# Optimization experiments

Measured on AMD Instinct MI355X. Metric: run time of the kernel, lower is better.

## Reference

```python
import jax, jax.numpy as jnp
import numpy as np

B, S, C = 2, 4096, 2048
H, D = 16, 128  # inner_dim = H*D = C
EPS = 1e-15     # processor self.eps
PAD_VAL = 1.0   # processor self.pad_val


def setup_inputs() -> dict:
    key = jax.random.key(0)
    ks = jax.random.split(key, 5)
    scale = C ** -0.5
    x = jax.random.normal(ks[0], (B, S, C), jnp.float32)
    Wq = jax.random.normal(ks[1], (C, C), jnp.float32) * scale
    Wk = jax.random.normal(ks[2], (C, C), jnp.float32) * scale
    Wv = jax.random.normal(ks[3], (C, C), jnp.float32) * scale
    Wo = jax.random.normal(ks[4], (C, C), jnp.float32) * scale
    bq = jnp.zeros((C,), jnp.float32)
    bk = jnp.zeros((C,), jnp.float32)
    bv = jnp.zeros((C,), jnp.float32)
    bo = jnp.zeros((C,), jnp.float32)
    # RoPE tables: pairs are adjacent (x.reshape(..., -1, 2)), so each freq repeats twice
    inv_freq = 1.0 / (10000.0 ** (np.arange(0, D, 2, dtype=np.float32) / D))
    freqs = np.outer(np.arange(S, dtype=np.float32), inv_freq)  # [S, D/2]
    emb = np.repeat(freqs, 2, axis=1)                            # [S, D]
    cos = jnp.asarray(np.cos(emb), jnp.float32)
    sin = jnp.asarray(np.sin(emb), jnp.float32)
    return {"x": x, "cos": cos, "sin": sin, "Wq": Wq, "bq": bq, "Wk": Wk,
            "bk": bk, "Wv": Wv, "bv": bv, "Wo": Wo, "bo": bo}


def _rope(t, cos, sin):
    # t: [B, H, S, D]; cos/sin: [S, D]; adjacent-pair rotation
    tr = t[..., 0::2]
    ti = t[..., 1::2]
    t_rot = jnp.stack([-ti, tr], axis=-1).reshape(t.shape)
    return t * cos + t_rot * sin


def reference(x, cos, sin, Wq, bq, Wk, bk, Wv, bv, Wo, bo):
    # projections -> [B, H, S, D] (matches transpose(-1,-2).reshape(B,H,D,S) split)
    q = (x @ Wq.T + bq).reshape(B, S, H, D).transpose(0, 2, 1, 3)
    k = (x @ Wk.T + bk).reshape(B, S, H, D).transpose(0, 2, 1, 3)
    v = (x @ Wv.T + bv).reshape(B, S, H, D).transpose(0, 2, 1, 3)
    # RoPE on q and k (self-attention), then ReLU feature map
    q = jax.nn.relu(_rope(q, cos, sin))
    k = jax.nn.relu(_rope(k, cos, sin))
    # pad value with ones along head_dim: torch F.pad(value,(0,0,0,1),value=1.0)
    v_pad = jnp.concatenate([v, jnp.full((B, H, S, 1), PAD_VAL, v.dtype)], axis=-1)  # [B,H,S,D+1]
    # linear attention: vk = value @ key  -> [B,H,D+1,D];  hs = vk @ query -> [B,H,D+1,S]
    vk = jnp.einsum('bhsn,bhsd->bhnd', v_pad, k)
    hs = jnp.einsum('bhnd,bhsd->bhns', vk, q)
    # eps-normalize by the padded-ones channel
    hs = hs[:, :, :-1] / (hs[:, :, -1:] + EPS)  # [B,H,D,S]
    out = hs.transpose(0, 3, 1, 2).reshape(B, S, H * D)  # view(B,H*D,S).permute(0,2,1)
    return out @ Wo.T + bo
```

## Files before the change

### kernel.cpp

```cpp
#include <hip/hip_runtime.h>


typedef unsigned short u16;
typedef __attribute__((ext_vector_type(8))) short bf16x8;
typedef __attribute__((ext_vector_type(4))) float f32x4;

__device__ __forceinline__ float bf2f(u16 u) {
    union { unsigned int i; float f; } x; x.i = ((unsigned int)u) << 16; return x.f;
}
__device__ __forceinline__ u16 f2bf(float f) {
    union { unsigned int i; float f; } x; x.f = f;
    unsigned int i = x.i;
    return (u16)((i + 0x7fffu + ((i >> 16) & 1u)) >> 16);
}
__device__ __forceinline__ uint4 pack8(const float* __restrict__ src) {
    float4 f0 = *(const float4*)(src);
    float4 f1 = *(const float4*)(src + 4);
    union { u16 u[8]; uint4 v; } P;
    P.u[0] = f2bf(f0.x); P.u[1] = f2bf(f0.y); P.u[2] = f2bf(f0.z); P.u[3] = f2bf(f0.w);
    P.u[4] = f2bf(f1.x); P.u[5] = f2bf(f1.y); P.u[6] = f2bf(f1.z); P.u[7] = f2bf(f1.w);
    return P.v;
}
__device__ __forceinline__ void gll16(void* lds, const void* g) {
    __builtin_amdgcn_global_load_lds(
        (const __attribute__((address_space(1))) unsigned int*)g,
        (__attribute__((address_space(3))) unsigned int*)lds, 16, 0, 0);
}

__global__ __launch_bounds__(256) void cast_all(
    const float* __restrict__ x,  const float* __restrict__ Wq,
    const float* __restrict__ Wk, const float* __restrict__ Wv,
    const float* __restrict__ Wo,
    u16* __restrict__ Xb, u16* __restrict__ Wqkvb, u16* __restrict__ Wob)
{
    int bid = blockIdx.x, t = threadIdx.x;
    const float* s; u16* d; size_t i;
    if (bid < 8192)       { s = x;  d = Xb;              i = (size_t)bid * 256 + t; }
    else if (bid < 10240) { s = Wq; d = Wqkvb;           i = (size_t)(bid - 8192)  * 256 + t; }
    else if (bid < 12288) { s = Wk; d = Wqkvb + 4194304; i = (size_t)(bid - 10240) * 256 + t; }
    else if (bid < 14336) { s = Wv; d = Wqkvb + 8388608; i = (size_t)(bid - 12288) * 256 + t; }
    else                  { s = Wo; d = Wob;             i = (size_t)(bid - 14336) * 256 + t; }
    *(uint4*)(d + i * 8) = pack8(s + i * 8);
}

__global__ __launch_bounds__(256) void gemm_qkv(
    const u16* __restrict__ Xb, const u16* __restrict__ Wqkvb,
    const float* __restrict__ bq, const float* __restrict__ bk, const float* __restrict__ bv,
    const float* __restrict__ cosT, const float* __restrict__ sinT,
    u16* __restrict__ Q, u16* __restrict__ K, u16* __restrict__ V)
{
    __shared__ __align__(16) u16 As[128 * 32];
    __shared__ __align__(16) u16 Bs[128 * 32];

    int t  = threadIdx.x;
    int bm = blockIdx.x;
    int bn = blockIdx.y;
    int region = bn >> 4;
    const u16*   W    = Wqkvb + (size_t)region * 4194304;
    const float* bias = (region == 0) ? bq : (region == 1 ? bk : bv);
    u16* OUT          = (region == 0) ? Q  : (region == 1 ? K  : V);

    int m0 = bm * 128;
    int n0 = (bn & 15) * 128;

    int w = t >> 6, lane = t & 63, quad = lane >> 4, l16 = lane & 15;
    int wm0 = (w >> 1) * 64, wn0 = (w & 1) * 64;
    int w32 = w * 32;
    int lr  = lane >> 2;
    int lc  = (lane & 3) * 8;

    const u16* ga = Xb + (size_t)(m0 + w32 + lr) * 2048 + lc;
    const u16* gb = W  + (size_t)(n0 + w32 + lr) * 2048 + lc;

    f32x4 acc[4][4] = {};

    for (int k0 = 0; k0 < 2048; k0 += 32) {
        __syncthreads();
        gll16(As + (size_t)w32 * 32,        ga + k0);
        gll16(As + (size_t)(w32 + 16) * 32, ga + k0 + 16 * 2048);
        gll16(Bs + (size_t)w32 * 32,        gb + k0);
        gll16(Bs + (size_t)(w32 + 16) * 32, gb + k0 + 16 * 2048);
        __syncthreads();

        bf16x8 af[4], bfr[4];
#pragma unroll
        for (int i = 0; i < 4; i++) af[i]  = *(const bf16x8*)(As + (wm0 + i * 16 + l16) * 32 + quad * 8);
#pragma unroll
        for (int j = 0; j < 4; j++) bfr[j] = *(const bf16x8*)(Bs + (wn0 + j * 16 + l16) * 32 + quad * 8);
#pragma unroll
        for (int i = 0; i < 4; i++)
#pragma unroll
            for (int j = 0; j < 4; j++)
                acc[i][j] = __builtin_amdgcn_mfma_f32_16x16x32_bf16(af[i], bfr[j], acc[i][j], 0, 0, 0);
    }

#pragma unroll
    for (int i = 0; i < 4; i++) {
#pragma unroll
        for (int j = 0; j < 4; j++) {
            int nc   = n0 + wn0 + j * 16 + l16;
            int h    = nc >> 7, dpos = nc & 127;
            float bia = bias[nc];
#pragma unroll
            for (int r = 0; r < 4; r++) {
                int mr = m0 + wm0 + i * 16 + quad * 4 + r;
                int b  = mr >> 12, s = mr & 4095;
                float val = acc[i][j][r] + bia;
                if (region < 2) {
                    float pair = __shfl_xor(val, 1, 64);
                    float c  = cosT[s * 128 + dpos];
                    float sn = sinT[s * 128 + dpos];
                    val = fmaxf(val * c + ((dpos & 1) ? pair : -pair) * sn, 0.f);
                }
                OUT[((size_t)(b * 16 + h) * 4096 + s) * 128 + dpos] = f2bf(val);
            }
        }
    }
}

__global__ __launch_bounds__(256) void ksum_kernel(
    const u16* __restrict__ Kb, float* __restrict__ ksumbuf)
{
    int bh = blockIdx.x, sc8 = blockIdx.y, t = threadIdx.x;
    int dpair = (t & 63) * 2, sq = t >> 6;
    const u16* base = Kb + (size_t)bh * 524288 + (size_t)(sc8 * 512 + sq * 128) * 128 + dpair;
    float s0 = 0.f, s1 = 0.f;
#pragma unroll 8
    for (int r = 0; r < 128; r++) {
        unsigned int wv = *(const unsigned int*)(base + (size_t)r * 128);
        s0 += bf2f((u16)(wv & 0xffff));
        s1 += bf2f((u16)(wv >> 16));
    }
    __shared__ float red[4][128];
    red[sq][dpair]     = s0;
    red[sq][dpair + 1] = s1;
    __syncthreads();
    if (t < 128) {
        float tot = red[0][t] + red[1][t] + red[2][t] + red[3][t];
        atomicAdd(&ksumbuf[bh * 128 + t], tot);
    }
}

__global__ __launch_bounds__(256) void vk_mfma(
    const u16* __restrict__ Kb, const u16* __restrict__ Vb, float* __restrict__ part)
{
    int bh = blockIdx.x;
    int sk = blockIdx.y;
    int t  = threadIdx.x;
    int s0 = sk * 512;

    __shared__ __align__(16) u16 Kt[128 * 32];
    __shared__ __align__(16) u16 Vt[128 * 32];

    const u16* Kp = Kb + (size_t)bh * 524288;
    const u16* Vp = Vb + (size_t)bh * 524288;

    int dgrp  = t & 15;
    int d0    = dgrp * 8;
    int spair = (t >> 4) * 2;
    int sg    = spair >> 3;

    int w = t >> 6, lane = t & 63, quad = lane >> 4, l16 = lane & 15;
    int nbase = (w >> 1) * 64, dbase = (w & 1) * 64;

    f32x4 acc[4][4] = {};

    for (int tile = 0; tile < 16; tile++) {
        int st = s0 + tile * 32;
        __syncthreads();
        {
            const u16* kg = Kp + (size_t)(st + spair) * 128 + d0;
            const u16* vg = Vp + (size_t)(st + spair) * 128 + d0;
            union { uint4 v; u16 u[8]; } ka, kb, va, vb;
            ka.v = *(const uint4*)kg;  kb.v = *(const uint4*)(kg + 128);
            va.v = *(const uint4*)vg;  vb.v = *(const uint4*)(vg + 128);
            int swz = (((sg + dgrp) & 3) << 3) + (spair & 7);
#pragma unroll
            for (int i = 0; i < 8; i++) {
                int e = (d0 + i) * 32 + swz;
                *(unsigned int*)(Kt + e) = (unsigned int)ka.u[i] | ((unsigned int)kb.u[i] << 16);
                *(unsigned int*)(Vt + e) = (unsigned int)va.u[i] | ((unsigned int)vb.u[i] << 16);
            }
        }
        __syncthreads();

        bf16x8 af[4], bfr[4];
#pragma unroll
        for (int i = 0; i < 4; i++) {
            int r = nbase + i * 16 + l16;
            af[i] = *(const bf16x8*)(Vt + r * 32 + (((quad + (r >> 3)) & 3) << 3));
        }
#pragma unroll
        for (int j = 0; j < 4; j++) {
            int r = dbase + j * 16 + l16;
            bfr[j] = *(const bf16x8*)(Kt + r * 32 + (((quad + (r >> 3)) & 3) << 3));
        }
#pragma unroll
        for (int i = 0; i < 4; i++)
#pragma unroll
            for (int j = 0; j < 4; j++)
                acc[i][j] = __builtin_amdgcn_mfma_f32_16x16x32_bf16(af[i], bfr[j], acc[i][j], 0, 0, 0);
    }

    float* dst = part + (size_t)(bh * 8 + sk) * 16384;
#pragma unroll
    for (int i = 0; i < 4; i++) {
#pragma unroll
        for (int j = 0; j < 4; j++) {
#pragma unroll
            for (int r = 0; r < 4; r++) {
                int n = nbase + i * 16 + quad * 4 + r;
                int d = dbase + j * 16 + l16;
                dst[n * 128 + d] = acc[i][j][r];
            }
        }
    }
}

__global__ __launch_bounds__(256) void vk_reduce(const float* __restrict__ part,
                                                 u16* __restrict__ vkb)
{
    int bh = blockIdx.x, by = blockIdx.y, t = threadIdx.x;
    int end = (by + 1) * 2048;
    for (int idx = by * 2048 + t; idx < end; idx += 256) {
        float s = 0.f;
#pragma unroll
        for (int p = 0; p < 8; p++) s += part[(size_t)(bh * 8 + p) * 16384 + idx];
        vkb[(size_t)bh * 16384 + idx] = f2bf(s);
    }
}

__global__ __launch_bounds__(256) void hs_mfma(
    const u16* __restrict__ Qb, const u16* __restrict__ vkb,
    const float* __restrict__ ksumbuf, u16* __restrict__ HS)
{
    int bh = blockIdx.x, sc = blockIdx.y;
    __shared__ __align__(16) u16 qL[128 * 136];
    __shared__ __align__(16) u16 vkL[128 * 136];
    __shared__ float rdL[128];
    __shared__ float ksumL[128];
    int t = threadIdx.x;

    const u16* Qp   = Qb  + ((size_t)bh * 4096 + sc * 128) * 128;
    const u16* vsrc = vkb + (size_t)bh * 16384;
    int row = t >> 4, colc = (t & 15) * 8;
#pragma unroll
    for (int r8 = 0; r8 < 8; r8++) {
        int rr = row + r8 * 16;
        *(uint4*)(qL  + rr * 136 + colc) = *(const uint4*)(Qp   + (size_t)rr * 128 + colc);
        *(uint4*)(vkL + rr * 136 + colc) = *(const uint4*)(vsrc + (size_t)rr * 128 + colc);
    }
    if (t < 128) ksumL[t] = ksumbuf[bh * 128 + t];
    __syncthreads();

    {
        int srow = t >> 1, half = t & 1;
        const u16*   q  = qL + srow * 136 + half * 64;
        const float* kp = ksumL + half * 64;
        float p = 0.f;
#pragma unroll 8
        for (int d = 0; d < 64; d += 4) {
            ushort4 qv = *(const ushort4*)(q + d);
            p += bf2f(qv.x) * kp[d] + bf2f(qv.y) * kp[d + 1]
               + bf2f(qv.z) * kp[d + 2] + bf2f(qv.w) * kp[d + 3];
        }
        p += __shfl_xor(p, 1, 64);
        if (half == 0) rdL[srow] = 1.0f / (p + 1e-15f);
    }

    int w = t >> 6, lane = t & 63, quad = lane >> 4, l16 = lane & 15;
    int wm0 = (w >> 1) * 64, wn0 = (w & 1) * 64;
    f32x4 acc[4][4] = {};
#pragma unroll
    for (int ks = 0; ks < 4; ks++) {
        bf16x8 af[4], bfr[4];
#pragma unroll
        for (int i = 0; i < 4; i++) af[i]  = *(const bf16x8*)(qL  + (wm0 + i * 16 + l16) * 136 + ks * 32 + quad * 8);
#pragma unroll
        for (int j = 0; j < 4; j++) bfr[j] = *(const bf16x8*)(vkL + (wn0 + j * 16 + l16) * 136 + ks * 32 + quad * 8);
#pragma unroll
        for (int i = 0; i < 4; i++)
#pragma unroll
            for (int j = 0; j < 4; j++)
                acc[i][j] = __builtin_amdgcn_mfma_f32_16x16x32_bf16(af[i], bfr[j], acc[i][j], 0, 0, 0);
    }
    __syncthreads();

    int b = bh >> 4, h = bh & 15;
#pragma unroll
    for (int i = 0; i < 4; i++) {
#pragma unroll
        for (int j = 0; j < 4; j++) {
#pragma unroll
            for (int r = 0; r < 4; r++) {
                int sl = wm0 + i * 16 + quad * 4 + r;
                int n  = wn0 + j * 16 + l16;
                size_t srow = (size_t)b * 4096 + sc * 128 + sl;
                HS[srow * 2048 + h * 128 + n] = f2bf(acc[i][j][r] * rdL[sl]);
            }
        }
    }
}

__global__ __launch_bounds__(256) void gemm_out(
    const u16* __restrict__ HSm, const u16* __restrict__ Wob,
    const float* __restrict__ bo, float* __restrict__ OUT)
{
    __shared__ __align__(16) u16 As[128 * 32];
    __shared__ __align__(16) u16 Bs[128 * 32];

    int t  = threadIdx.x;
    int m0 = blockIdx.x * 128;
    int n0 = blockIdx.y * 128;

    int w = t >> 6, lane = t & 63, quad = lane >> 4, l16 = lane & 15;
    int wm0 = (w >> 1) * 64, wn0 = (w & 1) * 64;
    int w32 = w * 32;
    int lr  = lane >> 2;
    int lc  = (lane & 3) * 8;

    const u16* ga = HSm + (size_t)(m0 + w32 + lr) * 2048 + lc;
    const u16* gb = Wob + (size_t)(n0 + w32 + lr) * 2048 + lc;

    f32x4 acc[4][4] = {};

    for (int k0 = 0; k0 < 2048; k0 += 32) {
        __syncthreads();
        gll16(As + (size_t)w32 * 32,        ga + k0);
        gll16(As + (size_t)(w32 + 16) * 32, ga + k0 + 16 * 2048);
        gll16(Bs + (size_t)w32 * 32,        gb + k0);
        gll16(Bs + (size_t)(w32 + 16) * 32, gb + k0 + 16 * 2048);
        __syncthreads();

        bf16x8 af[4], bfr[4];
#pragma unroll
        for (int i = 0; i < 4; i++) af[i]  = *(const bf16x8*)(As + (wm0 + i * 16 + l16) * 32 + quad * 8);
#pragma unroll
        for (int j = 0; j < 4; j++) bfr[j] = *(const bf16x8*)(Bs + (wn0 + j * 16 + l16) * 32 + quad * 8);
#pragma unroll
        for (int i = 0; i < 4; i++)
#pragma unroll
            for (int j = 0; j < 4; j++)
                acc[i][j] = __builtin_amdgcn_mfma_f32_16x16x32_bf16(af[i], bfr[j], acc[i][j], 0, 0, 0);
    }

#pragma unroll
    for (int i = 0; i < 4; i++) {
#pragma unroll
        for (int j = 0; j < 4; j++) {
            int nc = n0 + wn0 + j * 16 + l16;
            float bia = bo[nc];
#pragma unroll
            for (int r = 0; r < 4; r++) {
                int mr = m0 + wm0 + i * 16 + quad * 4 + r;
                OUT[(size_t)mr * 2048 + nc] = acc[i][j][r] + bia;
            }
        }
    }
}

extern "C" void kernel_launch(void* const* d_in, const int* in_sizes, int n_in,
                              void* d_out, int out_size, void* d_ws, size_t ws_size,
                              hipStream_t stream) {
    const float* x    = (const float*)d_in[0];
    const float* cosT = (const float*)d_in[1];
    const float* sinT = (const float*)d_in[2];
    const float* Wq   = (const float*)d_in[3];
    const float* bq   = (const float*)d_in[4];
    const float* Wk   = (const float*)d_in[5];
    const float* bk   = (const float*)d_in[6];
    const float* Wv   = (const float*)d_in[7];
    const float* bv   = (const float*)d_in[8];
    const float* Wo   = (const float*)d_in[9];
    const float* bo   = (const float*)d_in[10];

    char* ws = (char*)d_ws;
    u16*   Wqkvb   = (u16*)(ws);
    u16*   Wob     = (u16*)(ws + 25165824);
    u16*   Xb      = (u16*)(ws + 33554432);
    float* part    = (float*)(ws + 33554432);
    u16*   V       = (u16*)(ws + 67108864);
    u16*   HS      = V;
    u16*   vkb     = (u16*)(ws + 100663296);
    float* ksumbuf = (float*)(ws + 101711872);

    u16* Q  = (u16*)d_out;
    u16* Kb = (u16*)d_out + 16777216;

    hipMemsetAsync(ksumbuf, 0, 32 * 128 * sizeof(float), stream);
    cast_all<<<16384, 256, 0, stream>>>(x, Wq, Wk, Wv, Wo, Xb, Wqkvb, Wob);
    gemm_qkv<<<dim3(64, 48), 256, 0, stream>>>(Xb, Wqkvb, bq, bk, bv, cosT, sinT, Q, Kb, V);
    ksum_kernel<<<dim3(32, 8), 256, 0, stream>>>(Kb, ksumbuf);
    vk_mfma<<<dim3(32, 8), 256, 0, stream>>>(Kb, V, part);
    vk_reduce<<<dim3(32, 8), 256, 0, stream>>>(part, vkb);
    hs_mfma<<<dim3(32, 32), 256, 0, stream>>>(Q, vkb, ksumbuf, HS);
    gemm_out<<<dim3(64, 16), 256, 0, stream>>>(HS, Wob, bo, (float*)d_out);
}
```

Before: 587.8 us.

## Rewrite QKV and output GEMMs as 256x256 double-buffered pipelined MFMA kernels

Replaces the simple 128x128, K=32, two-barrier GEMM loops in gemm_qkv and gemm_out with a shared 256x256-tile, K=64 main loop run by 512 threads. The loop double-buffers LDS through global_load_lds, uses an XOR-swizzled LDS layout to avoid bank conflicts, interleaves the next tile's loads between MFMA phases with s_setprio, and remaps workgroup IDs to group tiles. The goal is to hide global-load latency and raise MFMA utilisation in the dominant GEMMs. The cost is 128KB of LDS and one workgroup per CU, plus a complex hand-tuned waitcnt and barrier schedule that is easy to get subtly wrong.

New measurement: 583.7 us. No clear change (-0.7%).

```diff
diff --git a/kernel.cpp b/kernel.cpp
--- a/kernel.cpp
+++ b/kernel.cpp
@@ -43,67 +43,155 @@
     *(uint4*)(d + i * 8) = pack8(s + i * 8);
 }
 
-__global__ __launch_bounds__(256) void gemm_qkv(
+__device__ __forceinline__ void mm256_loop(
+    const u16* __restrict__ gA, const u16* __restrict__ gB,
+    int w, int wm, int wn, int quad, int l16,
+    f32x4 (&acc)[8][4])
+{
+    __shared__ __align__(16) u16 As[2 * 16384];
+    __shared__ __align__(16) u16 Bs[2 * 16384];
+
+    const size_t CH = 64 * 2048;
+
+#define SGA(buf, c, koff) gll16(As + (buf) * 16384 + (c) * 4096 + w * 512, \
+                                gA + (size_t)(c) * CH + (koff))
+#define SGB(buf, c, koff) gll16(Bs + (buf) * 16384 + (c) * 4096 + w * 512, \
+                                gB + (size_t)(c) * CH + (koff))
+
+    SGA(0, 0, 0); SGA(0, 1, 0); SGA(0, 2, 0); SGA(0, 3, 0);
+    SGB(0, 0, 0); SGB(0, 1, 0); SGB(0, 2, 0); SGB(0, 3, 0);
+    SGB(1, 0, 64); SGB(1, 1, 64);
+    SGA(1, 0, 64); SGA(1, 1, 64); SGA(1, 2, 64); SGA(1, 3, 64);
+    asm volatile("s_waitcnt vmcnt(6)" ::: "memory");
+    __builtin_amdgcn_s_barrier();
+
+    const u16* A0 = As + wm * 8192;
+    const u16* B0 = Bs + wn * 4096;
+
+#pragma unroll 2
+    for (int t = 0; t < 32; ++t) {
+        const int buf = t & 1, nbuf = buf ^ 1;
+        const u16* Ab = A0 + buf * 16384;
+        const u16* Bb = B0 + buf * 16384;
+        const int k1 = (t + 1) * 64, k2 = (t + 2) * 64;
+
+        bf16x8 bF[4][2], aT[2][2];
+#pragma unroll
+        for (int n = 0; n < 4; n++)
+#pragma unroll
+            for (int kk = 0; kk < 2; kk++) {
+                int row = n * 16 + l16;
+                bF[n][kk] = *(const bf16x8*)(Bb + row * 64 + ((((kk << 2) + quad) ^ (row & 7)) << 3));
+            }
+#pragma unroll
+        for (int m = 0; m < 2; m++)
+#pragma unroll
+            for (int kk = 0; kk < 2; kk++) {
+                int row = m * 16 + l16;
+                aT[m][kk] = *(const bf16x8*)(Ab + row * 64 + ((((kk << 2) + quad) ^ (row & 7)) << 3));
+            }
+        if (t < 31) { SGB(nbuf, 2, k1); SGB(nbuf, 3, k1); }
+        __builtin_amdgcn_s_barrier();
+        asm volatile("s_waitcnt lgkmcnt(0)" ::: "memory");
+        __builtin_amdgcn_s_setprio(1);
+#pragma unroll
+        for (int m = 0; m < 2; m++)
+#pragma unroll
+            for (int n = 0; n < 4; n++)
+#pragma unroll
+                for (int kk = 0; kk < 2; kk++)
+                    acc[m][n] = __builtin_amdgcn_mfma_f32_16x16x32_bf16(aT[m][kk], bF[n][kk], acc[m][n], 0, 0, 0);
+        __builtin_amdgcn_s_setprio(0);
+        __builtin_amdgcn_s_barrier();
+
+        bf16x8 aR[6][2];
+#pragma unroll
+        for (int m = 0; m < 6; m++)
+#pragma unroll
+            for (int kk = 0; kk < 2; kk++) {
+                int row = (m + 2) * 16 + l16;
+                aR[m][kk] = *(const bf16x8*)(Ab + row * 64 + ((((kk << 2) + quad) ^ (row & 7)) << 3));
+            }
+        if (t < 30) { SGB(buf, 0, k2); SGB(buf, 1, k2); }
+        __builtin_amdgcn_s_barrier();
+        asm volatile("s_waitcnt lgkmcnt(0)" ::: "memory");
+        __builtin_amdgcn_s_setprio(1);
+#pragma unroll
+        for (int m = 0; m < 2; m++)
+#pragma unroll
+            for (int n = 0; n < 4; n++)
+#pragma unroll
+                for (int kk = 0; kk < 2; kk++)
+                    acc[2 + m][n] = __builtin_amdgcn_mfma_f32_16x16x32_bf16(aR[m][kk], bF[n][kk], acc[2 + m][n], 0, 0, 0);
+        __builtin_amdgcn_s_setprio(0);
+        __builtin_amdgcn_s_barrier();
+
+        if (t < 30) { SGA(buf, 0, k2); SGA(buf, 1, k2); }
+        __builtin_amdgcn_s_barrier();
+        __builtin_amdgcn_s_setprio(1);
+#pragma unroll
+        for (int m = 0; m < 2; m++)
+#pragma unroll
+            for (int n = 0; n < 4; n++)
+#pragma unroll
+                for (int kk = 0; kk < 2; kk++)
+                    acc[4 + m][n] = __builtin_amdgcn_mfma_f32_16x16x32_bf16(aR[2 + m][kk], bF[n][kk], acc[4 + m][n], 0, 0, 0);
+        __builtin_amdgcn_s_setprio(0);
+        __builtin_amdgcn_s_barrier();
+
+        if (t < 30) { SGA(buf, 2, k2); SGA(buf, 3, k2); }
+        __builtin_amdgcn_s_barrier();
+        __builtin_amdgcn_s_setprio(1);
+#pragma unroll
+        for (int m = 0; m < 2; m++)
+#pragma unroll
+            for (int n = 0; n < 4; n++)
+#pragma unroll
+                for (int kk = 0; kk < 2; kk++)
+                    acc[6 + m][n] = __builtin_amdgcn_mfma_f32_16x16x32_bf16(aR[4 + m][kk], bF[n][kk], acc[6 + m][n], 0, 0, 0);
+        __builtin_amdgcn_s_setprio(0);
+        if (t < 30)       asm volatile("s_waitcnt vmcnt(6)" ::: "memory");
+        else if (t == 30) asm volatile("s_waitcnt vmcnt(0)" ::: "memory");
+        __builtin_amdgcn_s_barrier();
+    }
+#undef SGA
+#undef SGB
+}
+
+__global__ __launch_bounds__(512, 1) void gemm_qkv(
     const u16* __restrict__ Xb, const u16* __restrict__ Wqkvb,
     const float* __restrict__ bq, const float* __restrict__ bk, const float* __restrict__ bv,
     const float* __restrict__ cosT, const float* __restrict__ sinT,
     u16* __restrict__ Q, u16* __restrict__ K, u16* __restrict__ V)
 {
-    __shared__ __align__(16) u16 As[128 * 32];
-    __shared__ __align__(16) u16 Bs[128 * 32];
-
-    int t  = threadIdx.x;
-    int bm = blockIdx.x;
-    int bn = blockIdx.y;
-    int region = bn >> 4;
+    int t = threadIdx.x, w = t >> 6, lane = t & 63, quad = lane >> 4, l16 = lane & 15;
+    int wm = w >> 2, wn = w & 3;
+
+    int wg = (blockIdx.x & 7) * 96 + (blockIdx.x >> 3);
+    int bm = wg & 31, bn = wg >> 5;
+    int region = bn >> 3;
     const u16*   W    = Wqkvb + (size_t)region * 4194304;
     const float* bias = (region == 0) ? bq : (region == 1 ? bk : bv);
     u16* OUT          = (region == 0) ? Q  : (region == 1 ? K  : V);
-
-    int m0 = bm * 128;
-    int n0 = (bn & 15) * 128;
-
-    int w = t >> 6, lane = t & 63, quad = lane >> 4, l16 = lane & 15;
-    int wm0 = (w >> 1) * 64, wn0 = (w & 1) * 64;
-    int w32 = w * 32;
-    int lr  = lane >> 2;
-    int lc  = (lane & 3) * 8;
-
-    const u16* ga = Xb + (size_t)(m0 + w32 + lr) * 2048 + lc;
-    const u16* gb = W  + (size_t)(n0 + w32 + lr) * 2048 + lc;
-
-    f32x4 acc[4][4] = {};
-
-    for (int k0 = 0; k0 < 2048; k0 += 32) {
-        __syncthreads();
-        gll16(As + (size_t)w32 * 32,        ga + k0);
-        gll16(As + (size_t)(w32 + 16) * 32, ga + k0 + 16 * 2048);
-        gll16(Bs + (size_t)w32 * 32,        gb + k0);
-        gll16(Bs + (size_t)(w32 + 16) * 32, gb + k0 + 16 * 2048);
-        __syncthreads();
-
-        bf16x8 af[4], bfr[4];
-#pragma unroll
-        for (int i = 0; i < 4; i++) af[i]  = *(const bf16x8*)(As + (wm0 + i * 16 + l16) * 32 + quad * 8);
-#pragma unroll
-        for (int j = 0; j < 4; j++) bfr[j] = *(const bf16x8*)(Bs + (wn0 + j * 16 + l16) * 32 + quad * 8);
-#pragma unroll
-        for (int i = 0; i < 4; i++)
-#pragma unroll
-            for (int j = 0; j < 4; j++)
-                acc[i][j] = __builtin_amdgcn_mfma_f32_16x16x32_bf16(af[i], bfr[j], acc[i][j], 0, 0, 0);
-    }
-
-#pragma unroll
-    for (int i = 0; i < 4; i++) {
+    int m0 = bm << 8, n0 = (bn & 7) << 8;
+
+    int lr8 = lane >> 3, lg = (lane & 7) ^ lr8;
+    const u16* gA = Xb + (size_t)(m0 + w * 8 + lr8) * 2048 + lg * 8;
+    const u16* gB = W  + (size_t)(n0 + w * 8 + lr8) * 2048 + lg * 8;
+
+    f32x4 acc[8][4] = {};
+    mm256_loop(gA, gB, w, wm, wn, quad, l16, acc);
+
+#pragma unroll
+    for (int i = 0; i < 8; i++) {
 #pragma unroll
         for (int j = 0; j < 4; j++) {
-            int nc   = n0 + wn0 + j * 16 + l16;
+            int nc   = n0 + wn * 64 + j * 16 + l16;
             int h    = nc >> 7, dpos = nc & 127;
             float bia = bias[nc];
 #pragma unroll
             for (int r = 0; r < 4; r++) {
-                int mr = m0 + wm0 + i * 16 + quad * 4 + r;
+                int mr = m0 + wm * 128 + i * 16 + quad * 4 + r;
                 int b  = mr >> 12, s = mr & 4095;
                 float val = acc[i][j][r] + bia;
                 if (region < 2) {
@@ -302,57 +390,33 @@
     }
 }
 
-__global__ __launch_bounds__(256) void gemm_out(
+__global__ __launch_bounds__(512, 1) void gemm_out(
     const u16* __restrict__ HSm, const u16* __restrict__ Wob,
     const float* __restrict__ bo, float* __restrict__ OUT)
 {
-    __shared__ __align__(16) u16 As[128 * 32];
-    __shared__ __align__(16) u16 Bs[128 * 32];
-
-    int t  = threadIdx.x;
-    int m0 = blockIdx.x * 128;
-    int n0 = blockIdx.y * 128;
-
-    int w = t >> 6, lane = t & 63, quad = lane >> 4, l16 = lane & 15;
-    int wm0 = (w >> 1) * 64, wn0 = (w & 1) * 64;
-    int w32 = w * 32;
-    int lr  = lane >> 2;
-    int lc  = (lane & 3) * 8;
-
-    const u16* ga = HSm + (size_t)(m0 + w32 + lr) * 2048 + lc;
-    const u16* gb = Wob + (size_t)(n0 + w32 + lr) * 2048 + lc;
-
-    f32x4 acc[4][4] = {};
-
-    for (int k0 = 0; k0 < 2048; k0 += 32) {
-        __syncthreads();
-        gll16(As + (size_t)w32 * 32,        ga + k0);
-        gll16(As + (size_t)(w32 + 16) * 32, ga + k0 + 16 * 2048);
-        gll16(Bs + (size_t)w32 * 32,        gb + k0);
-        gll16(Bs + (size_t)(w32 + 16) * 32, gb + k0 + 16 * 2048);
-        __syncthreads();
-
-        bf16x8 af[4], bfr[4];
-#pragma unroll
-        for (int i = 0; i < 4; i++) af[i]  = *(const bf16x8*)(As + (wm0 + i * 16 + l16) * 32 + quad * 8);
-#pragma unroll
-        for (int j = 0; j < 4; j++) bfr[j] = *(const bf16x8*)(Bs + (wn0 + j * 16 + l16) * 32 + quad * 8);
-#pragma unroll
-        for (int i = 0; i < 4; i++)
-#pragma unroll
-            for (int j = 0; j < 4; j++)
-                acc[i][j] = __builtin_amdgcn_mfma_f32_16x16x32_bf16(af[i], bfr[j], acc[i][j], 0, 0, 0);
-    }
-
-#pragma unroll
-    for (int i = 0; i < 4; i++) {
+    int t = threadIdx.x, w = t >> 6, lane = t & 63, quad = lane >> 4, l16 = lane & 15;
+    int wm = w >> 2, wn = w & 3;
+
+    int wg = (blockIdx.x & 7) * 32 + (blockIdx.x >> 3);
+    int bm = wg & 31, bn = wg >> 5;
+    int m0 = bm << 8, n0 = bn << 8;
+
+    int lr8 = lane >> 3, lg = (lane & 7) ^ lr8;
+    const u16* gA = HSm + (size_t)(m0 + w * 8 + lr8) * 2048 + lg * 8;
+    const u16* gB = Wob + (size_t)(n0 + w * 8 + lr8) * 2048 + lg * 8;
+
+    f32x4 acc[8][4] = {};
+    mm256_loop(gA, gB, w, wm, wn, quad, l16, acc);
+
+#pragma unroll
+    for (int i = 0; i < 8; i++) {
 #pragma unroll
         for (int j = 0; j < 4; j++) {
-            int nc = n0 + wn0 + j * 16 + l16;
+            int nc = n0 + wn * 64 + j * 16 + l16;
             float bia = bo[nc];
 #pragma unroll
             for (int r = 0; r < 4; r++) {
-                int mr = m0 + wm0 + i * 16 + quad * 4 + r;
+                int mr = m0 + wm * 128 + i * 16 + quad * 4 + r;
                 OUT[(size_t)mr * 2048 + nc] = acc[i][j][r] + bia;
             }
         }
@@ -389,10 +453,10 @@
 
     hipMemsetAsync(ksumbuf, 0, 32 * 128 * sizeof(float), stream);
     cast_all<<<16384, 256, 0, stream>>>(x, Wq, Wk, Wv, Wo, Xb, Wqkvb, Wob);
-    gemm_qkv<<<dim3(64, 48), 256, 0, stream>>>(Xb, Wqkvb, bq, bk, bv, cosT, sinT, Q, Kb, V);
+    gemm_qkv<<<768, 512, 0, stream>>>(Xb, Wqkvb, bq, bk, bv, cosT, sinT, Q, Kb, V);
     ksum_kernel<<<dim3(32, 8), 256, 0, stream>>>(Kb, ksumbuf);
     vk_mfma<<<dim3(32, 8), 256, 0, stream>>>(Kb, V, part);
     vk_reduce<<<dim3(32, 8), 256, 0, stream>>>(part, vkb);
     hs_mfma<<<dim3(32, 32), 256, 0, stream>>>(Q, vkb, ksumbuf, HS);
-    gemm_out<<<dim3(64, 16), 256, 0, stream>>>(HS, Wob, bo, (float*)d_out);
-}
+    gemm_out<<<256, 512, 0, stream>>>(HS, Wob, bo, (float*)d_out);
+}
```
